# Kernel optimization log

Measured on AMD Instinct MI355X. Metric: run time of the kernel, lower is better.

The kernel has to match this reference:

```python
import jax, jax.numpy as jnp
import numpy as np

N_NODES = 100000
N_EDGES = 1200000
D_FEAT = 64


def setup_inputs() -> dict:
    key = jax.random.key(0)
    k1, k2, k3 = jax.random.split(key, 3)
    feat = jax.random.normal(k1, (N_NODES, D_FEAT), dtype=jnp.float32)
    eps = jnp.zeros((1,), dtype=jnp.float32)
    edge_src = jax.random.randint(k2, (N_EDGES,), 0, N_NODES, dtype=jnp.int32)
    edge_dst = jax.random.randint(k3, (N_EDGES,), 0, N_NODES, dtype=jnp.int32)
    return {"feat": feat, "eps": eps, "edge_src": edge_src, "edge_dst": edge_dst}


def reference(feat, eps, edge_src, edge_dst):
    # DGL update_all(copy_u('h','m'), sum('m','neigh')):
    # gather source-node features along edges, segment-sum into destination nodes.
    messages = feat[edge_src]  # [E, D] gather
    neigh = jax.ops.segment_sum(messages, edge_dst, num_segments=N_NODES)  # [N, D]
    # eps-scaled residual: (1 + eps) * feat + neigh
    return (1.0 + eps) * feat + neigh
```

## Files before the change

### kernel.cpp

```cpp
#include <hip/hip_runtime.h>


#define N_NODES 100000
#define D_FEAT  64
#define N_EDGES 1200000

#define BSHIFT  6
#define NPB     64
#define KB      ((N_NODES + NPB - 1) / NPB)
#define CAP_B   1024
#define NCAP    32
#define OVL_CAP 128
#define CNT_STRIDE 16

#define PB       128
#define PTH      1024
#define EPB      ((N_EDGES + PB - 1) / PB)
#define B1       8
#define B2       8
#define CAST_ITEMS (N_NODES * D_FEAT / 8)
#define CAST_BLOCKS ((CAST_ITEMS + PTH - 1) / PTH)

__device__ __forceinline__ unsigned short f32_to_bf16_rne(float f) {
    unsigned int u = __float_as_uint(f);
    u += 0x7fffu + ((u >> 16) & 1u);
    return (unsigned short)(u >> 16);
}
__device__ __forceinline__ float bf_lo(unsigned int q) { return __uint_as_float(q << 16); }
__device__ __forceinline__ float bf_hi(unsigned int q) { return __uint_as_float(q & 0xffff0000u); }

__global__ __launch_bounds__(1024) void gin_cast_place_kernel(
    const float* __restrict__ feat,
    const int* __restrict__ edge_src,
    const int* __restrict__ edge_dst,
    unsigned int* __restrict__ fb,
    int* __restrict__ bcnt,
    int* __restrict__ buckets)
{
    const int tid = threadIdx.x;
    if (blockIdx.x < PB) {
        __shared__ int hist[KB];
        __shared__ int base[KB];
        __shared__ int lcur[KB];
        for (int k = tid; k < KB; k += PTH) { hist[k] = 0; lcur[k] = 0; }
        __syncthreads();

        const int e0 = blockIdx.x * EPB;
        const int e1 = min(e0 + EPB, N_EDGES);

        for (int e = e0 + tid; e < e1; e += PTH * B1) {
            int d[B1]; bool v[B1];
            #pragma unroll
            for (int u = 0; u < B1; ++u) {
                const int ee = e + u * PTH;
                v[u] = (ee < e1);
                if (v[u]) d[u] = edge_dst[ee];
            }
            #pragma unroll
            for (int u = 0; u < B1; ++u)
                if (v[u]) atomicAdd(&hist[d[u] >> BSHIFT], 1);
        }
        __syncthreads();

        for (int k = tid; k < KB; k += PTH) {
            const int h = hist[k];
            if (h > 0) base[k] = atomicAdd(&bcnt[k * CNT_STRIDE], h);
        }
        __syncthreads();

        for (int e = e0 + tid; e < e1; e += PTH * B2) {
            int d[B2], s[B2], t[B2]; bool v[B2];
            #pragma unroll
            for (int u = 0; u < B2; ++u) {
                const int ee = e + u * PTH;
                v[u] = (ee < e1);
                if (v[u]) { d[u] = edge_dst[ee]; s[u] = edge_src[ee]; }
            }
            #pragma unroll
            for (int u = 0; u < B2; ++u)
                if (v[u]) t[u] = base[d[u] >> BSHIFT] + atomicAdd(&lcur[d[u] >> BSHIFT], 1);
            #pragma unroll
            for (int u = 0; u < B2; ++u) {
                if (v[u]) {
                    const int k = d[u] >> BSHIFT;
                    if (t[u] < CAP_B)
                        buckets[k * CAP_B + t[u]] = s[u] | ((d[u] & (NPB - 1)) << 17);
                }
            }
        }
    } else {
        const int i = (blockIdx.x - PB) * PTH + tid;
        if (i < CAST_ITEMS) {
            const float4 f0 = reinterpret_cast<const float4*>(feat)[2 * i];
            const float4 f1 = reinterpret_cast<const float4*>(feat)[2 * i + 1];
            uint4 q;
            q.x = (unsigned)f32_to_bf16_rne(f0.x) | ((unsigned)f32_to_bf16_rne(f0.y) << 16);
            q.y = (unsigned)f32_to_bf16_rne(f0.z) | ((unsigned)f32_to_bf16_rne(f0.w) << 16);
            q.z = (unsigned)f32_to_bf16_rne(f1.x) | ((unsigned)f32_to_bf16_rne(f1.y) << 16);
            q.w = (unsigned)f32_to_bf16_rne(f1.z) | ((unsigned)f32_to_bf16_rne(f1.w) << 16);
            reinterpret_cast<uint4*>(fb)[i] = q;
        }
    }
}

__global__ __launch_bounds__(256) void gin_gather_kernel(
    const float* __restrict__ feat,
    const unsigned int* __restrict__ fb,
    const float* __restrict__ eps,
    const int* __restrict__ bcnt,
    const int* __restrict__ buckets,
    float* __restrict__ out)
{
    __shared__ int lcnt[NPB];
    __shared__ int sl[NPB * NCAP];
    __shared__ int2 ovl[OVL_CAP];
    __shared__ int ovl_n;
    const int tid  = threadIdx.x;
    const int k    = blockIdx.x;
    const int lane = tid & 63;
    const int w    = tid >> 6;

    if (tid < NPB) lcnt[tid] = 0;
    if (tid == 0) ovl_n = 0;
    __syncthreads();

    int m = bcnt[k * CNT_STRIDE];
    if (m > CAP_B) m = CAP_B;
    const int* __restrict__ bkt = buckets + k * CAP_B;
    for (int i = tid; i < m; i += 256) {
        const int e  = bkt[i];
        const int ld = e >> 17;
        const int t  = atomicAdd(&lcnt[ld], 1);
        if (t < NCAP) sl[ld * NCAP + t] = e & 0x1FFFF;
        else {
            const int o = atomicAdd(&ovl_n, 1);
            if (o < OVL_CAP) ovl[o] = make_int2(e & 0x1FFFF, ld);
        }
    }
    __syncthreads();

    const int r = lane >> 4;
    const int c = lane & 15;
    const float scale = 1.0f + eps[0];
    const int node_base = k * NPB;

    for (int nl = w * 16; nl < w * 16 + 16; nl += 2) {
        const int nodeA = node_base + nl;
        const int nodeB = nodeA + 1;
        int nA = lcnt[nl];     if (nA > NCAP) nA = NCAP;
        int nB = lcnt[nl + 1]; if (nB > NCAP) nB = NCAP;
        const int myA = sl[nl * NCAP + (lane & (NCAP - 1))];
        const int myB = sl[(nl + 1) * NCAP + (lane & (NCAP - 1))];

        float a0 = 0.f, a1 = 0.f, a2 = 0.f, a3 = 0.f;
        float b0 = 0.f, b1 = 0.f, b2 = 0.f, b3 = 0.f;
        const int nmax = (nA > nB) ? nA : nB;
        for (int j0 = 0; j0 < nmax; j0 += 4) {
            const int j  = j0 + r;
            const int jA = (j < nA) ? j : 0;
            const int jB = (j < nB) ? j : 0;
            const int sA = __shfl(myA, jA);
            const int sB = __shfl(myB, jB);
            if (j < nA) {
                const uint2 q = *reinterpret_cast<const uint2*>(&fb[sA * (D_FEAT / 2) + c * 2]);
                a0 += bf_lo(q.x); a1 += bf_hi(q.x);
                a2 += bf_lo(q.y); a3 += bf_hi(q.y);
            }
            if (j < nB) {
                const uint2 q = *reinterpret_cast<const uint2*>(&fb[sB * (D_FEAT / 2) + c * 2]);
                b0 += bf_lo(q.x); b1 += bf_hi(q.x);
                b2 += bf_lo(q.y); b3 += bf_hi(q.y);
            }
        }
        a0 += __shfl_xor(a0, 16); b0 += __shfl_xor(b0, 16);
        a1 += __shfl_xor(a1, 16); b1 += __shfl_xor(b1, 16);
        a2 += __shfl_xor(a2, 16); b2 += __shfl_xor(b2, 16);
        a3 += __shfl_xor(a3, 16); b3 += __shfl_xor(b3, 16);
        a0 += __shfl_xor(a0, 32); b0 += __shfl_xor(b0, 32);
        a1 += __shfl_xor(a1, 32); b1 += __shfl_xor(b1, 32);
        a2 += __shfl_xor(a2, 32); b2 += __shfl_xor(b2, 32);
        a3 += __shfl_xor(a3, 32); b3 += __shfl_xor(b3, 32);

        if (r == 0) {
            if (nodeA < N_NODES) {
                const float4 f = *reinterpret_cast<const float4*>(&feat[nodeA * D_FEAT + c * 4]);
                float4 o;
                o.x = scale * f.x + a0; o.y = scale * f.y + a1;
                o.z = scale * f.z + a2; o.w = scale * f.w + a3;
                *reinterpret_cast<float4*>(&out[nodeA * D_FEAT + c * 4]) = o;
            }
            if (nodeB < N_NODES) {
                const float4 f = *reinterpret_cast<const float4*>(&feat[nodeB * D_FEAT + c * 4]);
                float4 o;
                o.x = scale * f.x + b0; o.y = scale * f.y + b1;
                o.z = scale * f.z + b2; o.w = scale * f.w + b3;
                *reinterpret_cast<float4*>(&out[nodeB * D_FEAT + c * 4]) = o;
            }
        }
    }

    __syncthreads();
    int on = ovl_n; if (on > OVL_CAP) on = OVL_CAP;
    for (int i = w; i < on; i += 4) {
        const int2 ov = ovl[i];
        atomicAdd(&out[(node_base + ov.y) * D_FEAT + lane],
                  feat[ov.x * D_FEAT + lane]);
    }
}

__global__ __launch_bounds__(256) void gin_init_kernel(
    const float* __restrict__ feat, const float* __restrict__ eps, float* __restrict__ out)
{
    const float scale = 1.0f + eps[0];
    int i = blockIdx.x * blockDim.x + threadIdx.x;
    if (i < (N_NODES * D_FEAT) / 4) {
        float4 v = reinterpret_cast<const float4*>(feat)[i];
        v.x *= scale; v.y *= scale; v.z *= scale; v.w *= scale;
        reinterpret_cast<float4*>(out)[i] = v;
    }
}
__global__ __launch_bounds__(256) void gin_scatter_kernel(
    const float* __restrict__ feat, const int* __restrict__ edge_src,
    const int* __restrict__ edge_dst, float* __restrict__ out)
{
    const int edge = blockIdx.x * 4 + (threadIdx.x >> 6);
    const int lane = threadIdx.x & 63;
    if (edge < N_EDGES)
        atomicAdd(&out[edge_dst[edge] * D_FEAT + lane], feat[edge_src[edge] * D_FEAT + lane]);
}

extern "C" void kernel_launch(void* const* d_in, const int* in_sizes, int n_in,
                              void* d_out, int out_size, void* d_ws, size_t ws_size,
                              hipStream_t stream)
{
    const float* feat     = (const float*)d_in[0];
    const float* eps      = (const float*)d_in[1];
    const int*   edge_src = (const int*)d_in[2];
    const int*   edge_dst = (const int*)d_in[3];
    float* out = (float*)d_out;

    const size_t fb_ints   = (size_t)N_NODES * D_FEAT / 2;
    const size_t bcnt_ints = (size_t)KB * CNT_STRIDE;
    const size_t bkt_ints  = (size_t)KB * CAP_B;
    const size_t need = sizeof(int) * (fb_ints + bcnt_ints + bkt_ints);
    if (ws_size >= need) {
        unsigned int* fb = (unsigned int*)d_ws;
        int* bcnt    = (int*)(fb + fb_ints);
        int* buckets = bcnt + bcnt_ints;

        hipMemsetAsync(bcnt, 0, bcnt_ints * sizeof(int), stream);

        gin_cast_place_kernel<<<PB + CAST_BLOCKS, PTH, 0, stream>>>(
            feat, edge_src, edge_dst, fb, bcnt, buckets);
        gin_gather_kernel<<<KB, 256, 0, stream>>>(
            feat, fb, eps, bcnt, buckets, out);
    } else {
        const int total4 = (N_NODES * D_FEAT) / 4;
        gin_init_kernel<<<(total4 + 255) / 256, 256, 0, stream>>>(feat, eps, out);
        gin_scatter_kernel<<<(N_EDGES + 3) / 4, 256, 0, stream>>>(
            feat, edge_src, edge_dst, out);
    }
}
```

Before: 140.7 us.

## Accumulate bucket edges with LDS float atomics and load edges once

Result: slower. 556.0 us (+295.3%).

```diff
diff --git a/kernel.cpp b/kernel.cpp
--- a/kernel.cpp
+++ b/kernel.cpp
@@ -9,15 +9,13 @@
 #define NPB     64
 #define KB      ((N_NODES + NPB - 1) / NPB)
 #define CAP_B   1024
-#define NCAP    32
-#define OVL_CAP 128
 #define CNT_STRIDE 16
 
 #define PB       128
 #define PTH      1024
 #define EPB      ((N_EDGES + PB - 1) / PB)
-#define B1       8
-#define B2       8
+#define BN       10
+#define UB       8
 #define CAST_ITEMS (N_NODES * D_FEAT / 8)
 #define CAST_BLOCKS ((CAST_ITEMS + PTH - 1) / PTH)
 
@@ -48,18 +46,16 @@
         const int e0 = blockIdx.x * EPB;
         const int e1 = min(e0 + EPB, N_EDGES);
 
-        for (int e = e0 + tid; e < e1; e += PTH * B1) {
-            int d[B1]; bool v[B1];
-            #pragma unroll
-            for (int u = 0; u < B1; ++u) {
-                const int ee = e + u * PTH;
-                v[u] = (ee < e1);
-                if (v[u]) d[u] = edge_dst[ee];
-            }
-            #pragma unroll
-            for (int u = 0; u < B1; ++u)
-                if (v[u]) atomicAdd(&hist[d[u] >> BSHIFT], 1);
-        }
+        int d[BN], s[BN]; bool v[BN];
+        #pragma unroll
+        for (int u = 0; u < BN; ++u) {
+            const int ee = e0 + tid + u * PTH;
+            v[u] = (ee < e1);
+            if (v[u]) { d[u] = edge_dst[ee]; s[u] = edge_src[ee]; }
+        }
+        #pragma unroll
+        for (int u = 0; u < BN; ++u)
+            if (v[u]) atomicAdd(&hist[d[u] >> BSHIFT], 1);
         __syncthreads();
 
         for (int k = tid; k < KB; k += PTH) {
@@ -68,24 +64,16 @@
         }
         __syncthreads();
 
-        for (int e = e0 + tid; e < e1; e += PTH * B2) {
-            int d[B2], s[B2], t[B2]; bool v[B2];
-            #pragma unroll
-            for (int u = 0; u < B2; ++u) {
-                const int ee = e + u * PTH;
-                v[u] = (ee < e1);
-                if (v[u]) { d[u] = edge_dst[ee]; s[u] = edge_src[ee]; }
-            }
-            #pragma unroll
-            for (int u = 0; u < B2; ++u)
-                if (v[u]) t[u] = base[d[u] >> BSHIFT] + atomicAdd(&lcur[d[u] >> BSHIFT], 1);
-            #pragma unroll
-            for (int u = 0; u < B2; ++u) {
-                if (v[u]) {
-                    const int k = d[u] >> BSHIFT;
-                    if (t[u] < CAP_B)
-                        buckets[k * CAP_B + t[u]] = s[u] | ((d[u] & (NPB - 1)) << 17);
-                }
+        int t[BN];
+        #pragma unroll
+        for (int u = 0; u < BN; ++u)
+            if (v[u]) t[u] = base[d[u] >> BSHIFT] + atomicAdd(&lcur[d[u] >> BSHIFT], 1);
+        #pragma unroll
+        for (int u = 0; u < BN; ++u) {
+            if (v[u]) {
+                const int k = d[u] >> BSHIFT;
+                if (t[u] < CAP_B)
+                    buckets[k * CAP_B + t[u]] = s[u] | ((d[u] & (NPB - 1)) << 17);
             }
         }
     } else {
@@ -111,100 +99,62 @@
     const int* __restrict__ buckets,
     float* __restrict__ out)
 {
-    __shared__ int lcnt[NPB];
-    __shared__ int sl[NPB * NCAP];
-    __shared__ int2 ovl[OVL_CAP];
-    __shared__ int ovl_n;
+    __shared__ float accum[NPB * D_FEAT];
+    __shared__ int ent[CAP_B];
     const int tid  = threadIdx.x;
     const int k    = blockIdx.x;
     const int lane = tid & 63;
     const int w    = tid >> 6;
 
-    if (tid < NPB) lcnt[tid] = 0;
-    if (tid == 0) ovl_n = 0;
-    __syncthreads();
-
     int m = bcnt[k * CNT_STRIDE];
     if (m > CAP_B) m = CAP_B;
     const int* __restrict__ bkt = buckets + k * CAP_B;
-    for (int i = tid; i < m; i += 256) {
-        const int e  = bkt[i];
-        const int ld = e >> 17;
-        const int t  = atomicAdd(&lcnt[ld], 1);
-        if (t < NCAP) sl[ld * NCAP + t] = e & 0x1FFFF;
-        else {
-            const int o = atomicAdd(&ovl_n, 1);
-            if (o < OVL_CAP) ovl[o] = make_int2(e & 0x1FFFF, ld);
-        }
-    }
+    for (int i = tid; i < m; i += 256) ent[i] = bkt[i];
+    for (int i = tid; i < NPB * D_FEAT; i += 256) accum[i] = 0.f;
     __syncthreads();
 
-    const int r = lane >> 4;
-    const int c = lane & 15;
+    const int half = lane >> 5;
+    const int c    = lane & 31;
+
+    for (int p0 = w * 2 + half; p0 < m; p0 += 8 * UB) {
+        unsigned int q[UB]; int nd[UB]; bool vv[UB];
+        #pragma unroll
+        for (int u = 0; u < UB; ++u) {
+            const int p = p0 + u * 8;
+            vv[u] = (p < m);
+            if (vv[u]) {
+                const int e = ent[p];
+                nd[u] = e >> 17;
+                q[u]  = fb[(e & 0x1FFFF) * (D_FEAT / 2) + c];
+            }
+        }
+        #pragma unroll
+        for (int u = 0; u < UB; ++u) {
+            if (vv[u]) {
+                atomicAdd(&accum[nd[u] * D_FEAT + c],      bf_lo(q[u]));
+                atomicAdd(&accum[nd[u] * D_FEAT + 32 + c], bf_hi(q[u]));
+            }
+        }
+    }
+    __syncthreads();
+
     const float scale = 1.0f + eps[0];
     const int node_base = k * NPB;
-
-    for (int nl = w * 16; nl < w * 16 + 16; nl += 2) {
-        const int nodeA = node_base + nl;
-        const int nodeB = nodeA + 1;
-        int nA = lcnt[nl];     if (nA > NCAP) nA = NCAP;
-        int nB = lcnt[nl + 1]; if (nB > NCAP) nB = NCAP;
-        const int myA = sl[nl * NCAP + (lane & (NCAP - 1))];
-        const int myB = sl[(nl + 1) * NCAP + (lane & (NCAP - 1))];
-
-        float a0 = 0.f, a1 = 0.f, a2 = 0.f, a3 = 0.f;
-        float b0 = 0.f, b1 = 0.f, b2 = 0.f, b3 = 0.f;
-        const int nmax = (nA > nB) ? nA : nB;
-        for (int j0 = 0; j0 < nmax; j0 += 4) {
-            const int j  = j0 + r;
-            const int jA = (j < nA) ? j : 0;
-            const int jB = (j < nB) ? j : 0;
-            const int sA = __shfl(myA, jA);
-            const int sB = __shfl(myB, jB);
-            if (j < nA) {
-                const uint2 q = *reinterpret_cast<const uint2*>(&fb[sA * (D_FEAT / 2) + c * 2]);
-                a0 += bf_lo(q.x); a1 += bf_hi(q.x);
-                a2 += bf_lo(q.y); a3 += bf_hi(q.y);
-            }
-            if (j < nB) {
-                const uint2 q = *reinterpret_cast<const uint2*>(&fb[sB * (D_FEAT / 2) + c * 2]);
-                b0 += bf_lo(q.x); b1 += bf_hi(q.x);
-                b2 += bf_lo(q.y); b3 += bf_hi(q.y);
-            }
-        }
-        a0 += __shfl_xor(a0, 16); b0 += __shfl_xor(b0, 16);
-        a1 += __shfl_xor(a1, 16); b1 += __shfl_xor(b1, 16);
-        a2 += __shfl_xor(a2, 16); b2 += __shfl_xor(b2, 16);
-        a3 += __shfl_xor(a3, 16); b3 += __shfl_xor(b3, 16);
-        a0 += __shfl_xor(a0, 32); b0 += __shfl_xor(b0, 32);
-        a1 += __shfl_xor(a1, 32); b1 += __shfl_xor(b1, 32);
-        a2 += __shfl_xor(a2, 32); b2 += __shfl_xor(b2, 32);
-        a3 += __shfl_xor(a3, 32); b3 += __shfl_xor(b3, 32);
-
-        if (r == 0) {
-            if (nodeA < N_NODES) {
-                const float4 f = *reinterpret_cast<const float4*>(&feat[nodeA * D_FEAT + c * 4]);
-                float4 o;
-                o.x = scale * f.x + a0; o.y = scale * f.y + a1;
-                o.z = scale * f.z + a2; o.w = scale * f.w + a3;
-                *reinterpret_cast<float4*>(&out[nodeA * D_FEAT + c * 4]) = o;
-            }
-            if (nodeB < N_NODES) {
-                const float4 f = *reinterpret_cast<const float4*>(&feat[nodeB * D_FEAT + c * 4]);
-                float4 o;
-                o.x = scale * f.x + b0; o.y = scale * f.y + b1;
-                o.z = scale * f.z + b2; o.w = scale * f.w + b3;
-                *reinterpret_cast<float4*>(&out[nodeB * D_FEAT + c * 4]) = o;
-            }
-        }
-    }
-
-    __syncthreads();
-    int on = ovl_n; if (on > OVL_CAP) on = OVL_CAP;
-    for (int i = w; i < on; i += 4) {
-        const int2 ov = ovl[i];
-        atomicAdd(&out[(node_base + ov.y) * D_FEAT + lane],
-                  feat[ov.x * D_FEAT + lane]);
+    for (int i = tid; i < NPB * (D_FEAT / 4); i += 256) {
+        const int nl = i >> 4;
+        const int j  = i & 15;
+        const int node = node_base + nl;
+        if (node < N_NODES) {
+            const float4 f = *reinterpret_cast<const float4*>(&feat[node * D_FEAT + j * 4]);
+            const float s0 = accum[nl * D_FEAT + 2 * j];
+            const float s1 = accum[nl * D_FEAT + 2 * j + 32];
+            const float s2 = accum[nl * D_FEAT + 2 * j + 1];
+            const float s3 = accum[nl * D_FEAT + 2 * j + 33];
+            float4 o;
+            o.x = scale * f.x + s0; o.y = scale * f.y + s1;
+            o.z = scale * f.z + s2; o.w = scale * f.w + s3;
+            *reinterpret_cast<float4*>(&out[node * D_FEAT + j * 4]) = o;
+        }
     }
 }
 
```
